# Kernel optimization log

Hardware: AMD Instinct MI355X
Metric: run time of the kernel (lower is better)

Reference implementation:

```python
import jax, jax.numpy as jnp
import numpy as np
from jax import lax

B, H, W = 10, 320, 1024
PTS, DENSE, WD, KMEAN = 500, 2000, 11, 10
N = B * PTS  # 5000 center rows


def setup_inputs() -> dict:
    key = jax.random.key(0)
    k1, k2, k3, k4, k5, k6 = jax.random.split(key, 6)
    disp = jax.random.uniform(k1, (B, 1, H, W), dtype=jnp.float32)
    # forepred is a binary foreground prediction map -> strong Sobel edges
    forepred = jnp.round(jax.random.uniform(k2, (B, 1, H, W), dtype=jnp.float32))
    centerx = jax.random.randint(k3, (N,), WD, W - WD, dtype=jnp.int32)
    centery = jax.random.randint(k4, (N,), WD, H - WD, dtype=jnp.int32)
    bx = jax.random.randint(k5, (N, DENSE), -WD, WD + 1, dtype=jnp.int32)
    by = jax.random.randint(k6, (N, DENSE), -7, 8, dtype=jnp.int32)
    return {"disp": disp, "forepred": forepred, "centerx": centerx,
            "centery": centery, "bx": bx, "by": by}


def _mask_grad(disp, forepred):
    # Sobel-x conv, padding=1, no bias
    wx = jnp.array([[-1., 0., 1.], [-2., 0., 2.], [-1., 0., 1.]],
                   dtype=forepred.dtype)[None, None]  # [1,1,3,3]
    g = lax.conv_general_dilated(forepred, wx, (1, 1), 'SAME')
    mg = jnp.abs(g)
    # 3x3 max-pool, stride 1, padding 1 ("expand")
    mg = lax.reduce_window(mg, -jnp.inf, lax.max, (1, 1, 3, 3), (1, 1, 1, 1), 'SAME')
    mg = mg * (disp > 0.007).astype(mg.dtype)
    mg = jnp.maximum(mg, 3.0) - 3.0  # clamp(min=3) - 3
    # zero 4-pixel borders (zeroArea = [0,1,2,3,-1,-2,-3,-4])
    zy = jnp.array([0, 1, 2, 3, H - 1, H - 2, H - 3, H - 4])
    zx = jnp.array([0, 1, 2, 3, W - 1, W - 2, W - 3, W - 4])
    mg = mg.at[:, :, zy, :].set(0.0)
    mg = mg.at[:, :, :, zx].set(0.0)
    return mg


def reference(disp, forepred, centerx, centery, bx, by):
    maskGrad = _mask_grad(disp, forepred)
    channelInd = jnp.repeat(jnp.arange(B, dtype=jnp.int32), PTS)  # [N]
    # on-border row validity (original compacts; we mask instead, jit-friendly)
    validRow = maskGrad[channelInd, 0, centery, centerx] > 0.1  # [N]

    sampledx = centerx[:, None] + bx  # [N, DENSE]
    sampledy = centery[:, None] + by
    flat = (channelInd[:, None].astype(jnp.int32) * H + sampledy) * W + sampledx
    sampledDisp = disp.reshape(-1)[flat]  # irregular gather, [N, DENSE]

    kmeanLarge = jnp.max(sampledDisp, axis=1, keepdims=True)
    kmeanSmall = jnp.min(sampledDisp, axis=1, keepdims=True)
    for _ in range(KMEAN):
        distLarge = jnp.abs(sampledDisp - kmeanLarge)
        distSmall = jnp.abs(sampledDisp - kmeanSmall)
        belongingLarge = (distLarge <= distSmall).astype(sampledDisp.dtype)
        belongingSmall = 1.0 - belongingLarge
        kmeanLarge = (jnp.sum(sampledDisp * belongingLarge, axis=1, keepdims=True)
                      / jnp.sum(belongingLarge, axis=1, keepdims=True))
        kmeanSmall = (jnp.sum(sampledDisp * belongingSmall, axis=1, keepdims=True)
                      / jnp.sum(belongingSmall, axis=1, keepdims=True))

    contrast = ((kmeanLarge - kmeanSmall)[:, 0] > 0.005) & \
               (jnp.sum(belongingLarge, axis=1) > 5)
    keep = (validRow & contrast).astype(sampledDisp.dtype)  # [N]
    # per-row [large, small] cluster means; rows failing selection zeroed
    out = jnp.concatenate([kmeanLarge, kmeanSmall], axis=1) * keep[:, None]
    return out
```

## Files before the change

### kernel.cpp

```cpp
#include <hip/hip_runtime.h>

namespace {

constexpr int Bn    = 10;
constexpr int H     = 320;
constexpr int W     = 1024;
constexpr int PTS   = 500;
constexpr int DENSE = 2000;
constexpr int N     = Bn * PTS;
constexpr int HWp   = H * W;
constexpr int KITER = 10;

constexpr int WY   = 15;
constexpr int WX   = 24;
constexpr int WSZ  = WY * WX;
constexpr int WOFF = 7 * WX + 11;

__global__ __launch_bounds__(256, 8)
void rsbsp_kernel(const float* __restrict__ disp,
                  const float* __restrict__ forepred,
                  const int*   __restrict__ centerx,
                  const int*   __restrict__ centery,
                  const int*   __restrict__ bx,
                  const int*   __restrict__ by,
                  float*       __restrict__ out)
{
    __shared__ float ldsF[25];
    __shared__ float ldsG[9];
    __shared__ float win[WSZ];
    __shared__ float cmb0[4][3];
    __shared__ float cmb[2][4][2];

    const int t   = threadIdx.x;
    const int wid = t >> 6;
    const int row = blockIdx.x;
    const int b   = row / PTS;
    const int cx  = centerx[row];
    const int cy  = centery[row];
    const float* db = disp     + b * HWp;
    const float* fb = forepred + b * HWp;

    const float dcen = db[cy * W + cx];

    float fpix = 0.f;
    if (t < 25) {
        const int r = t / 5, c = t % 5;
        fpix = fb[(cy - 2 + r) * W + (cx - 2 + c)];
    }
    const int gbase = (cy - 7) * W + (cx - 11);
    float w0, w1 = 0.f;
    {
        const unsigned r0 = (unsigned)t / 24u, c0 = (unsigned)t - r0 * 24u;
        w0 = db[gbase + r0 * W + c0];
        const int i1 = t + 256;
        if (i1 < WSZ) {
            const unsigned r1 = (unsigned)i1 / 24u, c1 = (unsigned)i1 - r1 * 24u;
            w1 = db[gbase + r1 * W + c1];
        }
    }
    if (t < 25) ldsF[t] = fpix;
    win[t] = w0;
    if (t + 256 < WSZ) win[t + 256] = w1;
    __syncthreads();

    if (t < 9) {
        const int dy = t / 3, dx = t % 3;
        const float g =
                  (ldsF[(dy    ) * 5 + dx + 2] - ldsF[(dy    ) * 5 + dx])
           + 2.f * (ldsF[(dy + 1) * 5 + dx + 2] - ldsF[(dy + 1) * 5 + dx])
           +       (ldsF[(dy + 2) * 5 + dx + 2] - ldsF[(dy + 2) * 5 + dx]);
        ldsG[t] = fabsf(g);
    }
    __syncthreads();

    float v = 0.f;
    #pragma unroll
    for (int j = 0; j < 9; ++j) v = fmaxf(v, ldsG[j]);
    const float mgv = fmaxf(v * ((dcen > 0.007f) ? 1.f : 0.f), 3.f) - 3.f;
    const bool validRow = mgv > 0.1f;

    if (!validRow) {
        if (t == 0) { out[row * 2 + 0] = 0.f; out[row * 2 + 1] = 0.f; }
        return;
    }

    const int4* bx4 = reinterpret_cast<const int4*>(bx + row * DENSE);
    const int4* by4 = reinterpret_cast<const int4*>(by + row * DENSE);

    float s[8];
    float mx = -INFINITY, mn = INFINITY, tot = 0.f;
    #pragma unroll
    for (int k = 0; k < 2; ++k) {
        const int q = t + 256 * k;
        if (q < DENSE / 4) {
            const int4 xb = bx4[q];
            const int4 yb = by4[q];
            const float x0 = win[yb.x * WX + xb.x + WOFF];
            const float x1 = win[yb.y * WX + xb.y + WOFF];
            const float x2 = win[yb.z * WX + xb.z + WOFF];
            const float x3 = win[yb.w * WX + xb.w + WOFF];
            s[k * 4 + 0] = x0; s[k * 4 + 1] = x1;
            s[k * 4 + 2] = x2; s[k * 4 + 3] = x3;
            mx = fmaxf(fmaxf(fmaxf(mx, x0), fmaxf(x1, x2)), x3);
            mn = fminf(fminf(fminf(mn, x0), fminf(x1, x2)), x3);
            tot += (x0 + x1) + (x2 + x3);
        } else {
            s[k * 4 + 0] = -INFINITY; s[k * 4 + 1] = -INFINITY;
            s[k * 4 + 2] = -INFINITY; s[k * 4 + 3] = -INFINITY;
        }
    }

    #pragma unroll
    for (int m = 1; m < 64; m <<= 1) {
        mx  = fmaxf(mx, __shfl_xor(mx, m));
        mn  = fminf(mn, __shfl_xor(mn, m));
        tot += __shfl_xor(tot, m);
    }
    if ((t & 63) == 0) { cmb0[wid][0] = mx; cmb0[wid][1] = mn; cmb0[wid][2] = tot; }
    __syncthreads();
    mx  = fmaxf(fmaxf(cmb0[0][0], cmb0[1][0]), fmaxf(cmb0[2][0], cmb0[3][0]));
    mn  = fminf(fminf(cmb0[0][1], cmb0[1][1]), fminf(cmb0[2][1], cmb0[3][1]));
    tot = (cmb0[0][2] + cmb0[1][2]) + (cmb0[2][2] + cmb0[3][2]);

    float mL = mx, mS = mn;
    float cntLast = 0.f;
    float prevSum = -1.f, prevCnt = -1.f;
    #pragma unroll 1
    for (int it = 0; it < KITER; ++it) {
        const float mid = 0.5f * (mL + mS);
        float sumL = 0.f;
        int   cw   = 0;
        #pragma unroll
        for (int j = 0; j < 8; ++j) {
            const float x  = s[j];
            const bool  bl = x >= mid;
            sumL += bl ? x : 0.f;
            cw   += (int)__popcll(__ballot(bl));
        }
        #pragma unroll
        for (int m = 1; m < 64; m <<= 1) sumL += __shfl_xor(sumL, m);

        const int par = it & 1;
        if ((t & 63) == 0) { cmb[par][wid][0] = sumL; cmb[par][wid][1] = (float)cw; }
        __syncthreads();
        sumL = (cmb[par][0][0] + cmb[par][1][0]) + (cmb[par][2][0] + cmb[par][3][0]);
        const float cf = (cmb[par][0][1] + cmb[par][1][1]) + (cmb[par][2][1] + cmb[par][3][1]);
        const float df = (float)DENSE - cf;

        const bool done = (it == KITER - 1) || (cf == prevCnt && sumL == prevSum);
        if (done) {
            mL = sumL / cf;
            mS = (tot - sumL) / df;
            if (cf == (float)DENSE) mS = __int_as_float(0x7fc00000);
            cntLast = cf;
            break;
        }
        mL = sumL * __builtin_amdgcn_rcpf(cf);
        mS = (tot - sumL) * __builtin_amdgcn_rcpf(df);
        prevSum = sumL; prevCnt = cf;
    }

    if (t == 0) {
        const bool contrast = ((mL - mS) > 0.005f) && (cntLast > 5.f);
        const float keep = contrast ? 1.f : 0.f;
        out[row * 2 + 0] = mL * keep;
        out[row * 2 + 1] = mS * keep;
    }
}

}

extern "C" void kernel_launch(void* const* d_in, const int* in_sizes, int n_in,
                              void* d_out, int out_size, void* d_ws, size_t ws_size,
                              hipStream_t stream) {
    const float* disp = (const float*)d_in[0];
    const float* fore = (const float*)d_in[1];
    const int*   cx   = (const int*)d_in[2];
    const int*   cy   = (const int*)d_in[3];
    const int*   bxp  = (const int*)d_in[4];
    const int*   byp  = (const int*)d_in[5];
    float* out = (float*)d_out;

    rsbsp_kernel<<<N, 256, 0, stream>>>(disp, fore, cx, cy, bxp, byp, out);
}
```

Baseline: 125.4 us.

## Compute validity per-wave via shuffles and defer window load past early exit

Each wave now computes the 9 Sobel responses straight from global memory and reduces them with lane shuffles, which removes the two LDS staging buffers and two block barriers before the validity test. The disparity window load into LDS now happens after the early-exit check, so invalid rows skip it entirely. The bx/by index loads are issued before the window load so their latency overlaps it. The launch-bounds occupancy hint drops from 8 to 6 blocks. In exchange, every wave redoes the small forepred reads itself.

```diff
diff --git a/kernel.cpp b/kernel.cpp
--- a/kernel.cpp
+++ b/kernel.cpp
@@ -16,7 +16,7 @@
 constexpr int WSZ  = WY * WX;
 constexpr int WOFF = 7 * WX + 11;
 
-__global__ __launch_bounds__(256, 8)
+__global__ __launch_bounds__(256, 6)
 void rsbsp_kernel(const float* __restrict__ disp,
                   const float* __restrict__ forepred,
                   const int*   __restrict__ centerx,
@@ -25,58 +25,35 @@
                   const int*   __restrict__ by,
                   float*       __restrict__ out)
 {
-    __shared__ float ldsF[25];
-    __shared__ float ldsG[9];
     __shared__ float win[WSZ];
     __shared__ float cmb0[4][3];
     __shared__ float cmb[2][4][2];
 
-    const int t   = threadIdx.x;
-    const int wid = t >> 6;
-    const int row = blockIdx.x;
-    const int b   = row / PTS;
-    const int cx  = centerx[row];
-    const int cy  = centery[row];
+    const int t    = threadIdx.x;
+    const int wid  = t >> 6;
+    const int lane = t & 63;
+    const int row  = blockIdx.x;
+    const int b    = row / PTS;
+    const int cx   = centerx[row];
+    const int cy   = centery[row];
     const float* db = disp     + b * HWp;
     const float* fb = forepred + b * HWp;
 
+    float v = 0.f;
+    if (lane < 9) {
+        const int dy = lane / 3, dx = lane % 3;
+        const float* fp = fb + (cy - 2 + dy) * W + (cx - 2 + dx);
+        const float g = (fp[2]         - fp[0])
+                + 2.f * (fp[W + 2]     - fp[W])
+                +       (fp[2 * W + 2] - fp[2 * W]);
+        v = fabsf(g);
+    }
+    #pragma unroll
+    for (int m = 1; m < 16; m <<= 1) v = fmaxf(v, __shfl_xor(v, m));
+    v = __shfl(v, 0, 64);
+
     const float dcen = db[cy * W + cx];
-
-    float fpix = 0.f;
-    if (t < 25) {
-        const int r = t / 5, c = t % 5;
-        fpix = fb[(cy - 2 + r) * W + (cx - 2 + c)];
-    }
-    const int gbase = (cy - 7) * W + (cx - 11);
-    float w0, w1 = 0.f;
-    {
-        const unsigned r0 = (unsigned)t / 24u, c0 = (unsigned)t - r0 * 24u;
-        w0 = db[gbase + r0 * W + c0];
-        const int i1 = t + 256;
-        if (i1 < WSZ) {
-            const unsigned r1 = (unsigned)i1 / 24u, c1 = (unsigned)i1 - r1 * 24u;
-            w1 = db[gbase + r1 * W + c1];
-        }
-    }
-    if (t < 25) ldsF[t] = fpix;
-    win[t] = w0;
-    if (t + 256 < WSZ) win[t + 256] = w1;
-    __syncthreads();
-
-    if (t < 9) {
-        const int dy = t / 3, dx = t % 3;
-        const float g =
-                  (ldsF[(dy    ) * 5 + dx + 2] - ldsF[(dy    ) * 5 + dx])
-           + 2.f * (ldsF[(dy + 1) * 5 + dx + 2] - ldsF[(dy + 1) * 5 + dx])
-           +       (ldsF[(dy + 2) * 5 + dx + 2] - ldsF[(dy + 2) * 5 + dx]);
-        ldsG[t] = fabsf(g);
-    }
-    __syncthreads();
-
-    float v = 0.f;
-    #pragma unroll
-    for (int j = 0; j < 9; ++j) v = fmaxf(v, ldsG[j]);
-    const float mgv = fmaxf(v * ((dcen > 0.007f) ? 1.f : 0.f), 3.f) - 3.f;
+    const float mgv  = fmaxf(v * ((dcen > 0.007f) ? 1.f : 0.f), 3.f) - 3.f;
     const bool validRow = mgv > 0.1f;
 
     if (!validRow) {
@@ -86,28 +63,46 @@
 
     const int4* bx4 = reinterpret_cast<const int4*>(bx + row * DENSE);
     const int4* by4 = reinterpret_cast<const int4*>(by + row * DENSE);
+    int4 xb0 = make_int4(0, 0, 0, 0), yb0 = xb0, xb1 = xb0, yb1 = xb0;
+    xb0 = bx4[t]; yb0 = by4[t];
+    const bool q1on = (t + 256) < DENSE / 4;
+    if (q1on) { xb1 = bx4[t + 256]; yb1 = by4[t + 256]; }
+
+    const int gbase = (cy - 7) * W + (cx - 11);
+    {
+        const unsigned r0 = (unsigned)t / 24u, c0 = (unsigned)t - r0 * 24u;
+        win[t] = db[gbase + r0 * W + c0];
+        const int i1 = t + 256;
+        if (i1 < WSZ) {
+            const unsigned r1 = (unsigned)i1 / 24u, c1 = (unsigned)i1 - r1 * 24u;
+            win[i1] = db[gbase + r1 * W + c1];
+        }
+    }
+    __syncthreads();
 
     float s[8];
-    float mx = -INFINITY, mn = INFINITY, tot = 0.f;
-    #pragma unroll
-    for (int k = 0; k < 2; ++k) {
-        const int q = t + 256 * k;
-        if (q < DENSE / 4) {
-            const int4 xb = bx4[q];
-            const int4 yb = by4[q];
-            const float x0 = win[yb.x * WX + xb.x + WOFF];
-            const float x1 = win[yb.y * WX + xb.y + WOFF];
-            const float x2 = win[yb.z * WX + xb.z + WOFF];
-            const float x3 = win[yb.w * WX + xb.w + WOFF];
-            s[k * 4 + 0] = x0; s[k * 4 + 1] = x1;
-            s[k * 4 + 2] = x2; s[k * 4 + 3] = x3;
-            mx = fmaxf(fmaxf(fmaxf(mx, x0), fmaxf(x1, x2)), x3);
-            mn = fminf(fminf(fminf(mn, x0), fminf(x1, x2)), x3);
-            tot += (x0 + x1) + (x2 + x3);
-        } else {
-            s[k * 4 + 0] = -INFINITY; s[k * 4 + 1] = -INFINITY;
-            s[k * 4 + 2] = -INFINITY; s[k * 4 + 3] = -INFINITY;
-        }
+    float mx, mn, tot;
+    {
+        const float x0 = win[yb0.x * WX + xb0.x + WOFF];
+        const float x1 = win[yb0.y * WX + xb0.y + WOFF];
+        const float x2 = win[yb0.z * WX + xb0.z + WOFF];
+        const float x3 = win[yb0.w * WX + xb0.w + WOFF];
+        s[0] = x0; s[1] = x1; s[2] = x2; s[3] = x3;
+        mx = fmaxf(fmaxf(x0, x1), fmaxf(x2, x3));
+        mn = fminf(fminf(x0, x1), fminf(x2, x3));
+        tot = (x0 + x1) + (x2 + x3);
+    }
+    if (q1on) {
+        const float x0 = win[yb1.x * WX + xb1.x + WOFF];
+        const float x1 = win[yb1.y * WX + xb1.y + WOFF];
+        const float x2 = win[yb1.z * WX + xb1.z + WOFF];
+        const float x3 = win[yb1.w * WX + xb1.w + WOFF];
+        s[4] = x0; s[5] = x1; s[6] = x2; s[7] = x3;
+        mx = fmaxf(mx, fmaxf(fmaxf(x0, x1), fmaxf(x2, x3)));
+        mn = fminf(mn, fminf(fminf(x0, x1), fminf(x2, x3)));
+        tot += (x0 + x1) + (x2 + x3);
+    } else {
+        s[4] = -INFINITY; s[5] = -INFINITY; s[6] = -INFINITY; s[7] = -INFINITY;
     }
 
     #pragma unroll
@@ -116,7 +111,7 @@
         mn  = fminf(mn, __shfl_xor(mn, m));
         tot += __shfl_xor(tot, m);
     }
-    if ((t & 63) == 0) { cmb0[wid][0] = mx; cmb0[wid][1] = mn; cmb0[wid][2] = tot; }
+    if (lane == 0) { cmb0[wid][0] = mx; cmb0[wid][1] = mn; cmb0[wid][2] = tot; }
     __syncthreads();
     mx  = fmaxf(fmaxf(cmb0[0][0], cmb0[1][0]), fmaxf(cmb0[2][0], cmb0[3][0]));
     mn  = fminf(fminf(cmb0[0][1], cmb0[1][1]), fminf(cmb0[2][1], cmb0[3][1]));
@@ -141,7 +136,7 @@
         for (int m = 1; m < 64; m <<= 1) sumL += __shfl_xor(sumL, m);
 
         const int par = it & 1;
-        if ((t & 63) == 0) { cmb[par][wid][0] = sumL; cmb[par][wid][1] = (float)cw; }
+        if (lane == 0) { cmb[par][wid][0] = sumL; cmb[par][wid][1] = (float)cw; }
         __syncthreads();
         sumL = (cmb[par][0][0] + cmb[par][1][0]) + (cmb[par][2][0] + cmb[par][3][0]);
         const float cf = (cmb[par][0][1] + cmb[par][1][1]) + (cmb[par][2][1] + cmb[par][3][1]);
```

Result: no change. 126.5 us (+0.9%).
